# Optimization experiments

Hardware: AMD Instinct MI355X
Metric: run time of the kernel (lower is better)

## Reference

```python
import jax, jax.numpy as jnp
import numpy as np

C_IN = 128
C_OUT = 128
N_EDGE_TYPE = 7
N_NODE_TYPE = 7
AVG_DEGREE = 7
NUMD = 524288                 # nodes at depth d (multiple of 8)
LNUMD = 32768                 # leaf nodes at depth d-1
NNUM_DM1 = LNUMD + NUMD // 8  # 98304 nodes at depth d-1
PREFIX = 16384                # nodes at depths < d-1 kept in x
N_TOTAL_X = PREFIX + LNUMD + NUMD   # 573440
N_CONV = PREFIX + NNUM_DM1          # 114688 nodes seen by GraphConv
N_EDGES = N_CONV * AVG_DEGREE       # 802816


def setup_inputs() -> dict:
    key = jax.random.key(0)
    ks = jax.random.split(key, 6)
    x = jax.random.normal(ks[0], (N_TOTAL_X, C_IN), dtype=jnp.float32)
    # exactly LNUMD True entries (98304 = 3 * 32768), deterministic
    leaf_mask = (jnp.arange(NNUM_DM1) % 3) == 0
    edge_index = jax.random.randint(ks[1], (2, N_EDGES), 0, N_CONV)
    edge_type = jax.random.randint(ks[2], (N_EDGES,), 0, N_EDGE_TYPE)
    node_type = jax.random.randint(ks[3], (N_CONV,), 0, N_NODE_TYPE)
    w_down = jax.random.normal(ks[4], (C_IN, C_IN, 8), dtype=jnp.float32) * 0.02
    w_conv = jax.random.normal(
        ks[5], (N_EDGE_TYPE * (C_IN + N_NODE_TYPE), C_OUT), dtype=jnp.float32) * 0.02
    return dict(x=x, leaf_mask=leaf_mask, edge_index=edge_index,
                edge_type=edge_type, node_type=node_type,
                w_down=w_down, w_conv=w_conv)


def _graph_conv(x, edge_index, edge_type, node_type, w_conv):
    # x: [N, C]; augment with one-hot node type (n_node_type > 1)
    one_hot = jax.nn.one_hot(node_type, N_NODE_TYPE, dtype=x.dtype)
    xa = jnp.concatenate([x, one_hot], axis=1)          # [N, C+T]
    row, col = edge_index[0], edge_index[1]
    bucket = row * N_EDGE_TYPE + edge_type              # [E]
    # scatter-add neighbor features into per-(node, edge_type) buckets
    col_data = jax.ops.segment_sum(xa[col], bucket,
                                   num_segments=x.shape[0] * N_EDGE_TYPE)
    # [N, n_edge_type*(C+T)] @ [n_edge_type*(C+T), C_out]
    return col_data.reshape(x.shape[0], -1) @ w_conv


def reference(x, leaf_mask, edge_index, edge_type, node_type, w_down, w_conv):
    # Downsample: merge groups of 8 child nodes with a (C, C*8) weight
    xd = x[-NUMD:].reshape(-1, C_IN * 8)                # [NUMD/8, C*8]
    outd = xd @ w_down.reshape(C_IN, C_IN * 8).T        # [NUMD/8, C]
    # Masked scatter assembly: out[leaf_mask] = leaf feats, out[~mask] = outd
    x_leaf = x[-LNUMD - NUMD:-NUMD]                     # [LNUMD, C]
    li = jnp.cumsum(leaf_mask) - 1                      # position among leaves
    ni = jnp.cumsum(~leaf_mask) - 1                     # position among non-leaves
    merged = jnp.where(leaf_mask[:, None], x_leaf[li], outd[ni])  # [NNUM_DM1, C]
    out = jnp.concatenate([x[:-NUMD - LNUMD], merged], axis=0)    # [N_CONV, C]
    return _graph_conv(out, edge_index, edge_type, node_type, w_conv)
```

## Files before the change

### kernel.cpp

```cpp
#include <hip/hip_runtime.h>
#include <stdint.h>

#define C_IN 128
#define NUMD 524288
#define LNUMD 32768
#define NNUM_DM1 (LNUMD + NUMD/8)
#define PREFIX 16384
#define N_CONV (PREFIX + NNUM_DM1)
#define N_EDGES (N_CONV * 7)
#define ND8 (NUMD/8)
#define CAP 32
#define EG 12

#define COPY_BLK ((PREFIX+LNUMD)*32/256)
#define PREPW_N (114688 + 6272 + 131072)
#define PREPW_BLK ((PREPW_N + 255)/256)
#define ZERO_BLK (N_CONV/1024)
#define DOWN_BLK (ND8/128)
#define SCAT_BLK (N_EDGES/512)

typedef __attribute__((ext_vector_type(8))) short short8;
typedef __attribute__((ext_vector_type(4))) float f32x4;

__device__ inline ushort f2b(float f){
  union { float f; uint32_t u; } v; v.f = f;
  uint32_t r = v.u + 0x7fffu + ((v.u >> 16) & 1u);
  return (ushort)(r >> 16);
}
__device__ inline float b2f_lo(uint32_t u){ union { uint32_t u; float f; } v; v.u = u << 16; return v.f; }
__device__ inline float b2f_hi(uint32_t u){ union { uint32_t u; float f; } v; v.u = u & 0xffff0000u; return v.f; }

#define BAR_LGKM() do { \
    asm volatile("s_waitcnt lgkmcnt(0)" ::: "memory"); \
    __builtin_amdgcn_s_barrier(); \
    asm volatile("" ::: "memory"); \
  } while(0)

__global__ void k_prep(const float* __restrict__ x, const float* __restrict__ wconv,
                       const float* __restrict__ wdown,
                       ushort* __restrict__ xconv, ushort* __restrict__ w16y,
                       ushort* __restrict__ wbias, ushort* __restrict__ wd16,
                       int* __restrict__ cnt){
  const int bid = blockIdx.x;
  if (bid < COPY_BLK){
    int gid = bid*256 + threadIdx.x;
    int row = gid >> 5, seg = (gid & 31) * 4;
    int srow, drow;
    if (row < PREFIX){ srow = row; drow = row; }
    else { int k = row - PREFIX; srow = PREFIX + k; drow = PREFIX + 3*k; }
    const float4 f = *(const float4*)(x + (size_t)srow*C_IN + seg);
    ushort4 o; o.x=f2b(f.x); o.y=f2b(f.y); o.z=f2b(f.z); o.w=f2b(f.w);
    *(ushort4*)(xconv + (size_t)drow*C_IN + seg) = o;
  } else if (bid < COPY_BLK + PREPW_BLK){
    int gid = (bid - COPY_BLK)*256 + threadIdx.x;
    if (gid < 114688){
      int t = gid >> 14, rem = gid & 16383;
      int o = rem >> 7, k = rem & 127;
      w16y[gid] = f2b(wconv[(size_t)(t*135 + k)*128 + o]);
    } else if (gid < 120960){
      int q = gid - 114688;
      int t = q / 896, rem = q % 896;
      int n = rem >> 7, o = rem & 127;
      wbias[q] = f2b(wconv[(size_t)(t*135 + 128 + n)*128 + o]);
    } else if (gid < PREPW_N){
      int i = gid - 120960;
      wd16[i] = f2b(wdown[i]);
    }
  } else {
    int gid = (bid - COPY_BLK - PREPW_BLK)*256 + threadIdx.x;
    int4 z = {0,0,0,0};
    *(int4*)(cnt + gid*4) = z;
  }
}

__global__ __launch_bounds__(512) void k_sd(const int* __restrict__ ei, const int* __restrict__ et,
    int* __restrict__ cnt, int* __restrict__ bucket,
    const float* __restrict__ x, const ushort* __restrict__ wd16, ushort* __restrict__ xconv){
  const int bid = blockIdx.x;
  if (bid >= DOWN_BLK){
    int e = (bid - DOWN_BLK)*512 + threadIdx.x;
    int r = ei[e], c = ei[N_EDGES + e], t = et[e];
    int pos = atomicAdd(&cnt[r], 1);
    if (pos < CAP) bucket[r*CAP + pos] = c*7 + t;
    return;
  }
  __shared__ ushort As[128*128];
  const int tid = threadIdx.x;
  const int n0 = bid * 128;
  const float* xd = x + (size_t)(PREFIX+LNUMD)*C_IN;

  const int srow = tid >> 2, kbase = (tid & 3) * 32;
  const float* src = xd + (size_t)(n0+srow)*1024 + kbase;

  const int w = tid >> 6, l = tid & 63;
  const int mg = w >> 2, nc = w & 3;
  const int arow = l & 15, kgrp = l >> 4;
  const int obase = nc*32 + arow;

  f32x4 acc[4][2];
  #pragma unroll
  for (int mf=0;mf<4;mf++){ acc[mf][0]=(f32x4){0,0,0,0}; acc[mf][1]=(f32x4){0,0,0,0}; }

  float4 pf[8];
  #pragma unroll
  for (int i=0;i<8;i++) pf[i] = *(const float4*)(src + i*4);

  for (int c = 0; c < 8; ++c){
    #pragma unroll
    for (int i=0;i<4;i++){
      uint4 pk;
      pk.x = (uint)f2b(pf[2*i].x)   | ((uint)f2b(pf[2*i].y)<<16);
      pk.y = (uint)f2b(pf[2*i].z)   | ((uint)f2b(pf[2*i].w)<<16);
      pk.z = (uint)f2b(pf[2*i+1].x) | ((uint)f2b(pf[2*i+1].y)<<16);
      pk.w = (uint)f2b(pf[2*i+1].z) | ((uint)f2b(pf[2*i+1].w)<<16);
      int slot = (kbase >> 3) + i;
      *(uint4*)&As[srow*128 + ((slot ^ ((srow & 7) << 1)) << 3)] = pk;
    }
    BAR_LGKM();

    short8 breg[8];
    #pragma unroll
    for (int kf=0;kf<4;kf++){
      const ushort* bp = wd16 + c*128 + kf*32 + kgrp*8;
      breg[kf*2]   = *(const short8*)(bp + (size_t)obase*1024);
      breg[kf*2+1] = *(const short8*)(bp + (size_t)(obase+16)*1024);
    }
    if (c < 7){
      const float* s2 = src + (c+1)*128;
      #pragma unroll
      for (int i=0;i<8;i++) pf[i] = *(const float4*)(s2 + i*4);
    }

    #pragma unroll
    for (int kf=0;kf<4;kf++){
      #pragma unroll
      for (int mf=0;mf<4;mf++){
        int row = mg*64 + mf*16 + arow;
        int slot = (kf*4 + kgrp) ^ ((arow & 7) << 1);
        short8 a = *(const short8*)&As[row*128 + (slot << 3)];
        acc[mf][0] = __builtin_amdgcn_mfma_f32_16x16x32_bf16(a, breg[kf*2],   acc[mf][0], 0,0,0);
        acc[mf][1] = __builtin_amdgcn_mfma_f32_16x16x32_bf16(a, breg[kf*2+1], acc[mf][1], 0,0,0);
      }
    }
    BAR_LGKM();
  }

  #pragma unroll
  for (int mf = 0; mf < 4; ++mf){
    #pragma unroll
    for (int j = 0; j < 4; ++j){
      int rl = mg*64 + mf*16 + (l>>4)*4 + j;
      int n = n0 + rl;
      int i = 3*(n>>1) + 1 + (n&1);
      ushort* dst = xconv + (size_t)(PREFIX + i)*C_IN;
      dst[obase]      = f2b(acc[mf][0][j]);
      dst[obase + 16] = f2b(acc[mf][1][j]);
    }
  }
}

__global__ __launch_bounds__(512) void k_y(const ushort* __restrict__ xconv,
    const ushort* __restrict__ w16y, const ushort* __restrict__ wbias,
    const int* __restrict__ ntype, ushort* __restrict__ Y){
  __shared__ ushort As[128*128];
  __shared__ ushort bsh[6272];
  __shared__ int nts[128];
  const int tid = threadIdx.x;
  const int tile = blockIdx.x;

  {
    int row = tid >> 2;
    int c0 = (tid & 3) * 4;
    const ushort* src = xconv + ((size_t)tile*128 + row)*128;
    #pragma unroll
    for (int i=0;i<4;i++){
      int c16 = c0 + i;
      uint4 v = *(const uint4*)(src + c16*8);
      *(uint4*)&As[row*128 + ((c16 ^ (row & 7))*8)] = v;
    }
  }
  for (int i = tid; i < 3136; i += 512) ((uint*)bsh)[i] = ((const uint*)wbias)[i];
  if (tid < 128) nts[tid] = ntype[tile*128 + tid];
  __syncthreads();

  const int w = tid >> 6, l = tid & 63;
  const int mg = w >> 2, nc = w & 3;
  const int arow = l & 15, kgrp = l >> 4;
  const int obase = nc*32 + arow;

  for (int t = 0; t < 7; ++t){
    f32x4 acc[4][2];
    #pragma unroll
    for (int mf=0;mf<4;mf++){ acc[mf][0]=(f32x4){0,0,0,0}; acc[mf][1]=(f32x4){0,0,0,0}; }
    const ushort* wt = w16y + t*16384;
    #pragma unroll
    for (int kf = 0; kf < 4; ++kf){
      const int kof = kf*32 + kgrp*8;
      short8 b0 = *(const short8*)(wt + (size_t)obase*128 + kof);
      short8 b1 = *(const short8*)(wt + (size_t)(obase+16)*128 + kof);
      #pragma unroll
      for (int mf = 0; mf < 4; ++mf){
        int row = mg*64 + mf*16 + arow;
        int c16 = (kf*4 + kgrp) ^ (row & 7);
        short8 a = *(const short8*)&As[row*128 + c16*8];
        acc[mf][0] = __builtin_amdgcn_mfma_f32_16x16x32_bf16(a, b0, acc[mf][0], 0,0,0);
        acc[mf][1] = __builtin_amdgcn_mfma_f32_16x16x32_bf16(a, b1, acc[mf][1], 0,0,0);
      }
    }
    #pragma unroll
    for (int mf = 0; mf < 4; ++mf){
      #pragma unroll
      for (int j = 0; j < 4; ++j){
        int rl = mg*64 + mf*16 + (l>>4)*4 + j;
        int ntv = nts[rl];
        size_t grow = ((size_t)(tile*128 + rl)*7 + t)*128;
        int bb = (t*7 + ntv)*128;
        Y[grow + obase]      = f2b(acc[mf][0][j] + b2f_lo((uint)bsh[bb + obase]));
        Y[grow + obase + 16] = f2b(acc[mf][1][j] + b2f_lo((uint)bsh[bb + obase + 16]));
      }
    }
  }
}

__global__ __launch_bounds__(256) void k_gather(const int* __restrict__ cnt,
    const int* __restrict__ bucket, const ushort* __restrict__ Y, float* __restrict__ out){
  const int tid = threadIdx.x;
  const int slot = tid >> 5, lane = tid & 31;
  const int v = blockIdx.x*8 + slot;
  const int n = min(cnt[v], CAP);
  const int* brow = bucket + (size_t)v*CAP;
  float acc[4] = {0.f, 0.f, 0.f, 0.f};

  int m[EG]; uint2 d[EG];
  const int nb = min(n, EG);
  #pragma unroll
  for (int i=0;i<EG;i++) if (i < nb) m[i] = brow[i];
  #pragma unroll
  for (int i=0;i<EG;i++) if (i < nb)
    d[i] = *(const uint2*)(Y + (size_t)m[i]*C_IN + lane*4);
  #pragma unroll
  for (int i=0;i<EG;i++){
    if (i < nb){
      acc[0] += b2f_lo(d[i].x); acc[1] += b2f_hi(d[i].x);
      acc[2] += b2f_lo(d[i].y); acc[3] += b2f_hi(d[i].y);
    }
  }
  for (int e = EG; e < n; e += 4){
    int n4 = min(n - e, 4);
    int m4[4]; uint2 d4[4];
    #pragma unroll
    for (int i=0;i<4;i++) if (i < n4) m4[i] = brow[e + i];
    #pragma unroll
    for (int i=0;i<4;i++) if (i < n4)
      d4[i] = *(const uint2*)(Y + (size_t)m4[i]*C_IN + lane*4);
    #pragma unroll
    for (int i=0;i<4;i++){
      if (i < n4){
        acc[0] += b2f_lo(d4[i].x); acc[1] += b2f_hi(d4[i].x);
        acc[2] += b2f_lo(d4[i].y); acc[3] += b2f_hi(d4[i].y);
      }
    }
  }
  float4 o; o.x = acc[0]; o.y = acc[1]; o.z = acc[2]; o.w = acc[3];
  *(float4*)(out + (size_t)v*C_IN + lane*4) = o;
}

extern "C" void kernel_launch(void* const* d_in, const int* in_sizes, int n_in,
                              void* d_out, int out_size, void* d_ws, size_t ws_size,
                              hipStream_t stream){
  const float* x     = (const float*)d_in[0];
  const int*   ei    = (const int*)d_in[2];
  const int*   et    = (const int*)d_in[3];
  const int*   nt    = (const int*)d_in[4];
  const float* wdown = (const float*)d_in[5];
  const float* wconv = (const float*)d_in[6];
  float* out = (float*)d_out;

  char* p = (char*)d_ws;
  ushort* xconv = (ushort*)p; p += (size_t)N_CONV*C_IN*2;
  ushort* wd16  = (ushort*)p; p += (size_t)128*1024*2;
  ushort* w16y  = (ushort*)p; p += (size_t)114688*2;
  ushort* wbias = (ushort*)p; p += 16384;
  int* cnt      = (int*)p;    p += (size_t)N_CONV*4;
  int* bucket   = (int*)p;    p += (size_t)N_CONV*CAP*4;
  ushort* Y     = (ushort*)p;

  k_prep<<<COPY_BLK + PREPW_BLK + ZERO_BLK, 256, 0, stream>>>(x, wconv, wdown, xconv, w16y, wbias, wd16, cnt);
  k_sd<<<DOWN_BLK + SCAT_BLK, 512, 0, stream>>>(ei, et, cnt, bucket, x, wd16, xconv);
  k_y<<<N_CONV/128, 512, 0, stream>>>(xconv, w16y, wbias, nt, Y);
  k_gather<<<N_CONV/8, 256, 0, stream>>>(cnt, bucket, Y, out);
}
```

Baseline: 282.9 us.

## Skip Y stores for unreferenced node/edge-type rows and widen gather loads

During the edge scatter, a bitmap records which (column node, edge type) keys any edge references. The Y GEMM kernel reads that bitmap into shared memory and stores only the rows that will later be gathered, which cuts write traffic to the large bf16 Y buffer. The bitmap is cleared by extending the existing zeroing blocks, and it costs one extra global atomicOr per edge. Separately, the gather kernel now uses 16 lanes per node with 16-byte loads instead of 32 lanes with 8-byte loads.

Measured after the change: 327.4 us. 1.16x slower.

```diff
diff --git a/kernel.cpp b/kernel.cpp
--- a/kernel.cpp
+++ b/kernel.cpp
@@ -15,7 +15,7 @@
 #define COPY_BLK ((PREFIX+LNUMD)*32/256)
 #define PREPW_N (114688 + 6272 + 131072)
 #define PREPW_BLK ((PREPW_N + 255)/256)
-#define ZERO_BLK (N_CONV/1024)
+#define ZERO_BLK 137
 #define DOWN_BLK (ND8/128)
 #define SCAT_BLK (N_EDGES/512)
 
@@ -74,14 +74,16 @@
 }
 
 __global__ __launch_bounds__(512) void k_sd(const int* __restrict__ ei, const int* __restrict__ et,
-    int* __restrict__ cnt, int* __restrict__ bucket,
+    int* __restrict__ cnt, int* __restrict__ bucket, uint* __restrict__ bitmap,
     const float* __restrict__ x, const ushort* __restrict__ wd16, ushort* __restrict__ xconv){
   const int bid = blockIdx.x;
   if (bid >= DOWN_BLK){
     int e = (bid - DOWN_BLK)*512 + threadIdx.x;
     int r = ei[e], c = ei[N_EDGES + e], t = et[e];
+    int key = c*7 + t;
     int pos = atomicAdd(&cnt[r], 1);
-    if (pos < CAP) bucket[r*CAP + pos] = c*7 + t;
+    if (pos < CAP) bucket[r*CAP + pos] = key;
+    atomicOr(&bitmap[key >> 5], 1u << (key & 31));
     return;
   }
   __shared__ ushort As[128*128];
@@ -161,10 +163,12 @@
 
 __global__ __launch_bounds__(512) void k_y(const ushort* __restrict__ xconv,
     const ushort* __restrict__ w16y, const ushort* __restrict__ wbias,
-    const int* __restrict__ ntype, ushort* __restrict__ Y){
+    const int* __restrict__ ntype, const uint* __restrict__ bitmap,
+    ushort* __restrict__ Y){
   __shared__ ushort As[128*128];
   __shared__ ushort bsh[6272];
   __shared__ int nts[128];
+  __shared__ unsigned char usedb[896];
   const int tid = threadIdx.x;
   const int tile = blockIdx.x;
 
@@ -181,6 +185,10 @@
   }
   for (int i = tid; i < 3136; i += 512) ((uint*)bsh)[i] = ((const uint*)wbias)[i];
   if (tid < 128) nts[tid] = ntype[tile*128 + tid];
+  for (int i = tid; i < 896; i += 512){
+    int G = tile*896 + i;
+    usedb[i] = (bitmap[G >> 5] >> (G & 31)) & 1u;
+  }
   __syncthreads();
 
   const int w = tid >> 6, l = tid & 63;
@@ -212,11 +220,13 @@
       #pragma unroll
       for (int j = 0; j < 4; ++j){
         int rl = mg*64 + mf*16 + (l>>4)*4 + j;
-        int ntv = nts[rl];
-        size_t grow = ((size_t)(tile*128 + rl)*7 + t)*128;
-        int bb = (t*7 + ntv)*128;
-        Y[grow + obase]      = f2b(acc[mf][0][j] + b2f_lo((uint)bsh[bb + obase]));
-        Y[grow + obase + 16] = f2b(acc[mf][1][j] + b2f_lo((uint)bsh[bb + obase + 16]));
+        if (usedb[rl*7 + t]){
+          int ntv = nts[rl];
+          size_t grow = ((size_t)(tile*128 + rl)*7 + t)*128;
+          int bb = (t*7 + ntv)*128;
+          Y[grow + obase]      = f2b(acc[mf][0][j] + b2f_lo((uint)bsh[bb + obase]));
+          Y[grow + obase + 16] = f2b(acc[mf][1][j] + b2f_lo((uint)bsh[bb + obase + 16]));
+        }
       }
     }
   }
@@ -225,44 +235,51 @@
 __global__ __launch_bounds__(256) void k_gather(const int* __restrict__ cnt,
     const int* __restrict__ bucket, const ushort* __restrict__ Y, float* __restrict__ out){
   const int tid = threadIdx.x;
-  const int slot = tid >> 5, lane = tid & 31;
-  const int v = blockIdx.x*8 + slot;
+  const int slot = tid >> 4, lane = tid & 15;
+  const int v = blockIdx.x*16 + slot;
   const int n = min(cnt[v], CAP);
   const int* brow = bucket + (size_t)v*CAP;
-  float acc[4] = {0.f, 0.f, 0.f, 0.f};
-
-  int m[EG]; uint2 d[EG];
+  float acc[8] = {0.f,0.f,0.f,0.f,0.f,0.f,0.f,0.f};
+
+  int m[EG]; uint4 d[EG];
   const int nb = min(n, EG);
   #pragma unroll
   for (int i=0;i<EG;i++) if (i < nb) m[i] = brow[i];
   #pragma unroll
   for (int i=0;i<EG;i++) if (i < nb)
-    d[i] = *(const uint2*)(Y + (size_t)m[i]*C_IN + lane*4);
+    d[i] = *(const uint4*)(Y + (size_t)m[i]*C_IN + lane*8);
   #pragma unroll
   for (int i=0;i<EG;i++){
     if (i < nb){
       acc[0] += b2f_lo(d[i].x); acc[1] += b2f_hi(d[i].x);
       acc[2] += b2f_lo(d[i].y); acc[3] += b2f_hi(d[i].y);
+      acc[4] += b2f_lo(d[i].z); acc[5] += b2f_hi(d[i].z);
+      acc[6] += b2f_lo(d[i].w); acc[7] += b2f_hi(d[i].w);
     }
   }
   for (int e = EG; e < n; e += 4){
     int n4 = min(n - e, 4);
-    int m4[4]; uint2 d4[4];
+    int m4[4]; uint4 d4[4];
     #pragma unroll
     for (int i=0;i<4;i++) if (i < n4) m4[i] = brow[e + i];
     #pragma unroll
     for (int i=0;i<4;i++) if (i < n4)
-      d4[i] = *(const uint2*)(Y + (size_t)m4[i]*C_IN + lane*4);
+      d4[i] = *(const uint4*)(Y + (size_t)m4[i]*C_IN + lane*8);
     #pragma unroll
     for (int i=0;i<4;i++){
       if (i < n4){
         acc[0] += b2f_lo(d4[i].x); acc[1] += b2f_hi(d4[i].x);
         acc[2] += b2f_lo(d4[i].y); acc[3] += b2f_hi(d4[i].y);
+        acc[4] += b2f_lo(d4[i].z); acc[5] += b2f_hi(d4[i].z);
+        acc[6] += b2f_lo(d4[i].w); acc[7] += b2f_hi(d4[i].w);
       }
     }
   }
-  float4 o; o.x = acc[0]; o.y = acc[1]; o.z = acc[2]; o.w = acc[3];
-  *(float4*)(out + (size_t)v*C_IN + lane*4) = o;
+  float4 o0; o0.x=acc[0]; o0.y=acc[1]; o0.z=acc[2]; o0.w=acc[3];
+  float4 o1; o1.x=acc[4]; o1.y=acc[5]; o1.z=acc[6]; o1.w=acc[7];
+  float* dst = out + (size_t)v*C_IN + lane*8;
+  *(float4*)dst = o0;
+  *(float4*)(dst + 4) = o1;
 }
 
 extern "C" void kernel_launch(void* const* d_in, const int* in_sizes, int n_in,
@@ -282,11 +299,12 @@
   ushort* w16y  = (ushort*)p; p += (size_t)114688*2;
   ushort* wbias = (ushort*)p; p += 16384;
   int* cnt      = (int*)p;    p += (size_t)N_CONV*4;
+  uint* bitmap  = (uint*)p;   p += 25600*4;
   int* bucket   = (int*)p;    p += (size_t)N_CONV*CAP*4;
   ushort* Y     = (ushort*)p;
 
   k_prep<<<COPY_BLK + PREPW_BLK + ZERO_BLK, 256, 0, stream>>>(x, wconv, wdown, xconv, w16y, wbias, wd16, cnt);
-  k_sd<<<DOWN_BLK + SCAT_BLK, 512, 0, stream>>>(ei, et, cnt, bucket, x, wd16, xconv);
-  k_y<<<N_CONV/128, 512, 0, stream>>>(xconv, w16y, wbias, nt, Y);
-  k_gather<<<N_CONV/8, 256, 0, stream>>>(cnt, bucket, Y, out);
-}
+  k_sd<<<DOWN_BLK + SCAT_BLK, 512, 0, stream>>>(ei, et, cnt, bucket, bitmap, x, wd16, xconv);
+  k_y<<<N_CONV/128, 512, 0, stream>>>(xconv, w16y, wbias, nt, bitmap, Y);
+  k_gather<<<N_CONV/16, 256, 0, stream>>>(cnt, bucket, Y, out);
+}
```
